# Performance work log

Measured on AMD Instinct MI355X. Metric: run time of the kernel, lower is better.

Reference implementation:

```python
import jax, jax.numpy as jnp
import numpy as np

D_MODEL = 512
N_HEADS = 8
HEAD_DIM = D_MODEL // N_HEADS
BATCH = 2
SEQ = 4096
MAX_SEQ = 4096


def _rope_tables(max_len, dim):
    # freqs = 1/10000^(arange(0,dim,2)/dim); outer(t, freqs); polar -> cos/sin
    inv = 1.0 / (10000.0 ** (np.arange(0, dim, 2, dtype=np.float32) / dim))
    t = np.arange(max_len, dtype=np.float32)
    ang = np.outer(t, inv)  # [max_len, dim/2]
    return jnp.asarray(np.cos(ang)), jnp.asarray(np.sin(ang))


def _apply_rope(x, cos, sin):
    # x: [B, S, H, Hd]; complex-pair rotation over last dim pairs
    B, S, H, Hd = x.shape
    xr = x.reshape(B, S, H, Hd // 2, 2)
    xe, xo = xr[..., 0], xr[..., 1]
    c = cos[:S][None, :, None, :]  # [1,S,1,Hd/2]
    s = sin[:S][None, :, None, :]
    re = xe * c - xo * s
    im = xe * s + xo * c
    return jnp.stack([re, im], axis=-1).reshape(B, S, H, Hd)


def setup_inputs() -> dict:
    key = jax.random.key(0)
    kx, kq, kk, kv, ko = jax.random.split(key, 5)
    std = 1.0 / np.sqrt(D_MODEL)
    return {
        "x": jax.random.normal(kx, (BATCH, SEQ, D_MODEL), dtype=jnp.float32),
        "Wq": jax.random.normal(kq, (D_MODEL, D_MODEL), dtype=jnp.float32) * std,
        "Wk": jax.random.normal(kk, (D_MODEL, D_MODEL), dtype=jnp.float32) * std,
        "Wv": jax.random.normal(kv, (D_MODEL, D_MODEL), dtype=jnp.float32) * std,
        "Wo": jax.random.normal(ko, (D_MODEL, D_MODEL), dtype=jnp.float32) * std,
    }


def reference(x, Wq, Wk, Wv, Wo):
    B, S, D = x.shape
    cos, sin = _rope_tables(MAX_SEQ, HEAD_DIM)
    # nn.Linear: y = x @ W.T
    q = (x @ Wq.T).reshape(B, S, N_HEADS, HEAD_DIM)
    k = (x @ Wk.T).reshape(B, S, N_HEADS, HEAD_DIM)
    v = (x @ Wv.T).reshape(B, S, N_HEADS, HEAD_DIM)
    q = _apply_rope(q, cos, sin)
    k = _apply_rope(k, cos, sin)
    scale = HEAD_DIM ** (-0.5)
    # [B,H,S,S]
    scores = jnp.einsum("bshd,bthd->bhst", q, k) * scale
    causal = jnp.tril(jnp.ones((S, S), dtype=bool))
    scores = jnp.where(causal[None, None], scores, -jnp.inf)
    attn = jax.nn.softmax(scores, axis=-1)
    out = jnp.einsum("bhst,bthd->bshd", attn, v).reshape(B, S, D)
    return out @ Wo.T
```

## Files before the change

kernel.cpp:

```cpp
#include <hip/hip_runtime.h>
#include <hip/hip_bf16.h>
#include <math.h>

#define D_MODEL 512
#define N_HEADS 8
#define HEAD_DIM 64
#define BATCH 2
#define SEQ 4096
#define M_ROWS (BATCH*SEQ)

typedef __attribute__((ext_vector_type(8))) short short8;
typedef __attribute__((ext_vector_type(4))) float f32x4;

__device__ inline short f2bf(float f) {
  union { float f; unsigned u; } v; v.f = f;
  unsigned u = v.u;
  unsigned r = u + 0x7FFFu + ((u >> 16) & 1u);
  return (short)(r >> 16);
}
__device__ inline float bf2f(short s) {
  union { unsigned u; float f; } v; v.u = ((unsigned)(unsigned short)s) << 16;
  return v.f;
}

__device__ inline void gll16(const void* g, void* l) {
  __builtin_amdgcn_global_load_lds(
      (const __attribute__((address_space(1))) unsigned int*)g,
      (__attribute__((address_space(3))) unsigned int*)l, 16, 0, 0);
}

__device__ inline short8 cvt8(float4 a, float4 b) {
  short8 o;
  o[0] = f2bf(a.x); o[1] = f2bf(a.y); o[2] = f2bf(a.z); o[3] = f2bf(a.w);
  o[4] = f2bf(b.x); o[5] = f2bf(b.y); o[6] = f2bf(b.z); o[7] = f2bf(b.w);
  return o;
}

#define XOCT (M_ROWS*D_MODEL/8)
#define WOCT (3*D_MODEL*D_MODEL/8)
#define OOCT (D_MODEL*D_MODEL/8)
__global__ void prep_kernel(const float* __restrict__ x,
                            const float* __restrict__ Wq,
                            const float* __restrict__ Wk,
                            const float* __restrict__ Wv,
                            const float* __restrict__ Wo,
                            short* __restrict__ xb,
                            short* __restrict__ Wqkv,
                            short* __restrict__ Wob,
                            float* __restrict__ cosT,
                            float* __restrict__ sinT) {
  int i = blockIdx.x * blockDim.x + threadIdx.x;
  if (i < XOCT) {
    float4 a = *(const float4*)&x[i * 8];
    float4 b = *(const float4*)&x[i * 8 + 4];
    *(short8*)&xb[i * 8] = cvt8(a, b);
  }
  if (i < WOCT) {
    int e = i * 8;
    int t = e >> 18, r = e & 262143;
    const float* W = (t == 0) ? Wq : ((t == 1) ? Wk : Wv);
    float4 a = *(const float4*)&W[r];
    float4 b = *(const float4*)&W[r + 4];
    *(short8*)&Wqkv[e] = cvt8(a, b);
  }
  if (i < OOCT) {
    float4 a = *(const float4*)&Wo[i * 8];
    float4 b = *(const float4*)&Wo[i * 8 + 4];
    *(short8*)&Wob[i * 8] = cvt8(a, b);
  }
  if (i < SEQ * 32) {
    int s = i >> 5, p = i & 31;
    float e = (float)(2 * p) * (1.0f / 64.0f);
    float inv = powf(10000.0f, -e);
    float ang = (float)s * inv;
    float sv, cv;
    sincosf(ang, &sv, &cv);
    cosT[i] = cv; sinT[i] = sv;
  }
}

template<int MODE>
__global__ __launch_bounds__(256) void gemm_kernel(const short* __restrict__ A,
                                                   const short* __restrict__ B,
                                                   float* __restrict__ out_f,
                                                   short* __restrict__ Qb,
                                                   short* __restrict__ Kb,
                                                   short* __restrict__ Vb,
                                                   const float* __restrict__ cosT,
                                                   const float* __restrict__ sinT) {
  __shared__ short smem[128 * 72 * 2];
  short (*As)[72] = (short(*)[72])smem;
  short (*Bs)[72] = (short(*)[72])(smem + 128 * 72);
  short (*Cs)[136] = (short(*)[136])smem;

  const int m0 = blockIdx.x * 128;
  const int n0 = blockIdx.y * 128;
  const int tid = threadIdx.x;
  const int lane = tid & 63, wid = tid >> 6;
  const int wm = wid >> 1, wn = wid & 1;
  const int l15 = lane & 15, g = lane >> 4;
  const int Kdim = 512;

  f32x4 acc[4][4] = {};

  for (int kt = 0; kt < Kdim; kt += 64) {
    __syncthreads();
    for (int it = 0; it < 4; ++it) {
      int c = it * 256 + tid;
      int row = c >> 3, col = (c & 7) << 3;
      *(short8*)&As[row][col] = *(const short8*)&A[(m0 + row) * Kdim + kt + col];
      *(short8*)&Bs[row][col] = *(const short8*)&B[(n0 + row) * Kdim + kt + col];
    }
    __syncthreads();
    for (int kk = 0; kk < 64; kk += 32) {
      short8 a[4], b[4];
      for (int mi = 0; mi < 4; ++mi)
        a[mi] = *(const short8*)&As[wm * 64 + mi * 16 + l15][kk + (g << 3)];
      for (int ni = 0; ni < 4; ++ni)
        b[ni] = *(const short8*)&Bs[wn * 64 + ni * 16 + l15][kk + (g << 3)];
      for (int mi = 0; mi < 4; ++mi)
        for (int ni = 0; ni < 4; ++ni)
          acc[mi][ni] = __builtin_amdgcn_mfma_f32_16x16x32_bf16(a[mi], b[ni], acc[mi][ni], 0, 0, 0);
    }
  }

  if (MODE == 1) {
    for (int mi = 0; mi < 4; ++mi)
      for (int ni = 0; ni < 4; ++ni)
        for (int r = 0; r < 4; ++r) {
          int row_g = m0 + wm * 64 + mi * 16 + (g << 2) + r;
          int col_g = n0 + wn * 64 + ni * 16 + l15;
          out_f[row_g * 512 + col_g] = acc[mi][ni][r];
        }
    return;
  }

  const int t_blk = n0 >> 9;
  __syncthreads();

  if (t_blk < 2) {
    const float qs = (t_blk == 0) ? 0.18033688011112042f : 1.0f;
    for (int mi = 0; mi < 4; ++mi)
      for (int ni = 0; ni < 4; ++ni)
        for (int r = 0; r < 4; ++r) {
          int lrow = wm * 64 + mi * 16 + (g << 2) + r;
          int ss = (m0 + lrow) & 4095;
          int d = (n0 + wn * 64 + ni * 16 + l15) & 63;
          int p = d >> 1;
          float c = cosT[ss * 32 + p], s = sinT[ss * 32 + p];
          float v = acc[mi][ni][r];
          float partner = __shfl_xor(v, 1);
          float res = (l15 & 1) ? (v * c + partner * s) : (v * c - partner * s);
          Cs[lrow][wn * 64 + ni * 16 + l15] = f2bf(res * qs);
        }
  } else {
    for (int mi = 0; mi < 4; ++mi)
      for (int ni = 0; ni < 4; ++ni)
        for (int r = 0; r < 4; ++r)
          Cs[wm * 64 + mi * 16 + (g << 2) + r][wn * 64 + ni * 16 + l15] =
              f2bf(acc[mi][ni][r]);
  }
  __syncthreads();

  if (t_blk < 2) {
    short* dst = (t_blk == 0) ? Qb : Kb;
#pragma unroll
    for (int it = 0; it < 8; ++it) {
      int row = (tid >> 4) + (it << 4);
      int colb = (tid & 15) << 3;
      short8 vv = *(const short8*)&Cs[row][colb];
      int row_g = m0 + row;
      int ss = row_g & 4095, bb = row_g >> 12;
      int cc = (n0 + colb) & 511;
      int h = cc >> 6, d = cc & 63;
      *(short8*)&dst[(((bb << 3) + h) * SEQ + ss) * 64 + d] = vv;
    }
  } else {
#pragma unroll
    for (int it = 0; it < 8; ++it) {
      int c = tid & 127;
      int sb = ((tid >> 7) << 3) + (it << 4);
      short8 o8;
#pragma unroll
      for (int j = 0; j < 8; ++j) o8[j] = Cs[sb + j][c];
      int row_g0 = m0 + sb;
      int ss = row_g0 & 4095, bb = row_g0 >> 12;
      int cc = (n0 + c) & 511;
      int h = cc >> 6, d = cc & 63;
      *(short8*)&Vb[((long)(((bb << 3) + h) * 64 + d)) * SEQ + ss] = o8;
    }
  }
}

__global__ __launch_bounds__(512, 4) void attn_kernel(const short* __restrict__ Q,
                                                      const short* __restrict__ K,
                                                      const short* __restrict__ Vt,
                                                      short* __restrict__ O) {
  __shared__ short Ks[2][64 * 64];
  __shared__ short Vs[2][64 * 64];
  __shared__ short P_lds[8][16][72];

  const int o = blockIdx.x;
  const int j = o >> 4;
  const int bh = o & 15;
  const int tile = (o < 256) ? (31 - j) : (j - 16);

  const int tid = threadIdx.x, lane = tid & 63, w = tid >> 6;
  const int l15 = lane & 15, g = lane >> 4;
  const long base = (long)bh * SEQ * 64;
  const long baseV = (long)bh * 64 * SEQ;
  const int bb = bh >> 3, h = bh & 7;

  const int srow = tid >> 3;
  const int sc16k = (tid & 7) ^ (srow & 7);
  short* ldsSegK0 = &Ks[0][(tid >> 6) << 9];
  short* ldsSegK1 = &Ks[1][(tid >> 6) << 9];
  short* ldsSegV0 = &Vs[0][(tid >> 6) << 9];
  short* ldsSegV1 = &Vs[1][(tid >> 6) << 9];

  const int q0 = (tile << 7) + (w << 4);
  const int nc = 2 * tile + 2;

  short8 aq0 = *(const short8*)&Q[base + (long)(q0 + l15) * 64 + (g << 3)];
  short8 aq1 = *(const short8*)&Q[base + (long)(q0 + l15) * 64 + 32 + (g << 3)];

  f32x4 o_acc[4] = {};
  float m_r[4], l_r[4];
#pragma unroll
  for (int r = 0; r < 4; ++r) { m_r[r] = -__builtin_inff(); l_r[r] = 0.f; }

  gll16(&K[base + (long)srow * 64 + sc16k * 8], ldsSegK0);
  gll16(&Vt[baseV + (long)srow * SEQ + sc16k * 8], ldsSegV0);

  for (int c = 0; c < nc; ++c) {
    const int kv0 = c << 6;
    const int bi = c & 1;
    __syncthreads();
    if (c + 1 < nc) {
      const int nkv = (c + 1) << 6;
      short* dK = (bi ? ldsSegK0 : ldsSegK1);
      short* dV = (bi ? ldsSegV0 : ldsSegV1);
      gll16(&K[base + (long)(nkv + srow) * 64 + sc16k * 8], dK);
      gll16(&Vt[baseV + (long)srow * SEQ + nkv + sc16k * 8], dV);
    }
    if (kv0 > q0) continue;

    f32x4 sf[4] = {};
    __builtin_amdgcn_s_setprio(1);
#pragma unroll
    for (int f = 0; f < 4; ++f) {
      int row = f * 16 + l15, sw = row & 7;
      short8 bk0 = *(const short8*)&Ks[bi][row * 64 + ((g) ^ sw) * 8];
      short8 bk1 = *(const short8*)&Ks[bi][row * 64 + ((4 + g) ^ sw) * 8];
      sf[f] = __builtin_amdgcn_mfma_f32_16x16x32_bf16(aq0, bk0, sf[f], 0, 0, 0);
      sf[f] = __builtin_amdgcn_mfma_f32_16x16x32_bf16(aq1, bk1, sf[f], 0, 0, 0);
    }
    __builtin_amdgcn_s_setprio(0);
    if (kv0 == (q0 & ~63)) {
#pragma unroll
      for (int f = 0; f < 4; ++f) {
        int kvc = kv0 + f * 16 + l15;
#pragma unroll
        for (int r = 0; r < 4; ++r) {
          int qrow = q0 + (g << 2) + r;
          if (kvc > qrow) sf[f][r] = -__builtin_inff();
        }
      }
    }

    float pmx[4];
#pragma unroll
    for (int r = 0; r < 4; ++r)
      pmx[r] = fmaxf(fmaxf(sf[0][r], sf[1][r]), fmaxf(sf[2][r], sf[3][r]));
    bool ok = (pmx[0] <= m_r[0] + 8.f) && (pmx[1] <= m_r[1] + 8.f) &&
              (pmx[2] <= m_r[2] + 8.f) && (pmx[3] <= m_r[3] + 8.f);
    if (!__all(ok)) {
      float pm[4];
#pragma unroll
      for (int r = 0; r < 4; ++r) pm[r] = pmx[r];
#pragma unroll
      for (int off = 1; off < 16; off <<= 1)
#pragma unroll
        for (int r = 0; r < 4; ++r)
          pm[r] = fmaxf(pm[r], __shfl_xor(pm[r], off));
#pragma unroll
      for (int r = 0; r < 4; ++r) {
        float mn = fmaxf(m_r[r], pm[r]);
        float alpha = exp2f(m_r[r] - mn);
        m_r[r] = mn;
        l_r[r] *= alpha;
#pragma unroll
        for (int db = 0; db < 4; ++db) o_acc[db][r] *= alpha;
      }
    }

    float pr[4][4];
#pragma unroll
    for (int r = 0; r < 4; ++r)
#pragma unroll
      for (int f = 0; f < 4; ++f) {
        float pv = exp2f(sf[f][r] - m_r[r]);
        pr[f][r] = pv;
        l_r[r] += pv;
      }

#pragma unroll
    for (int f = 0; f < 4; ++f)
#pragma unroll
      for (int r = 0; r < 4; ++r)
        P_lds[w][(g << 2) + r][f * 16 + l15] = f2bf(pr[f][r]);

    short8 pa0 = *(const short8*)&P_lds[w][l15][(g << 3)];
    short8 pa1 = *(const short8*)&P_lds[w][l15][32 + (g << 3)];

    __builtin_amdgcn_s_setprio(1);
#pragma unroll
    for (int kk = 0; kk < 2; ++kk) {
      short8 pa = kk ? pa1 : pa0;
#pragma unroll
      for (int db = 0; db < 4; ++db) {
        int row = db * 16 + l15, sw = row & 7;
        short8 bv = *(const short8*)&Vs[bi][row * 64 + ((kk * 4 + g) ^ sw) * 8];
        o_acc[db] = __builtin_amdgcn_mfma_f32_16x16x32_bf16(pa, bv, o_acc[db], 0, 0, 0);
      }
    }
    __builtin_amdgcn_s_setprio(0);
  }

#pragma unroll
  for (int off = 1; off < 16; off <<= 1)
#pragma unroll
    for (int r = 0; r < 4; ++r)
      l_r[r] += __shfl_xor(l_r[r], off);

#pragma unroll
  for (int db = 0; db < 4; ++db)
#pragma unroll
    for (int r = 0; r < 4; ++r) {
      int s_g = q0 + (g << 2) + r;
      float v = o_acc[db][r] / l_r[r];
      O[((long)(bb * SEQ + s_g)) * 512 + h * 64 + db * 16 + l15] = f2bf(v);
    }
}

extern "C" void kernel_launch(void* const* d_in, const int* in_sizes, int n_in,
                              void* d_out, int out_size, void* d_ws, size_t ws_size,
                              hipStream_t stream) {
  const float* x  = (const float*)d_in[0];
  const float* Wq = (const float*)d_in[1];
  const float* Wk = (const float*)d_in[2];
  const float* Wv = (const float*)d_in[3];
  const float* Wo = (const float*)d_in[4];

  char* ws = (char*)d_ws;
  size_t off = 0;
  auto alloc = [&](size_t bytes) {
    void* p = ws + off;
    off += (bytes + 255) & ~(size_t)255;
    return p;
  };
  short* xb   = (short*)alloc((size_t)M_ROWS * 512 * 2);
  short* Wqkv = (short*)alloc((size_t)1536 * 512 * 2);
  short* Wob  = (short*)alloc((size_t)512 * 512 * 2);
  float* cosT = (float*)alloc((size_t)SEQ * 32 * 4);
  float* sinT = (float*)alloc((size_t)SEQ * 32 * 4);
  short* Qb   = (short*)alloc((size_t)16 * SEQ * 64 * 2);
  short* Kb   = (short*)alloc((size_t)16 * SEQ * 64 * 2);
  short* Vt   = (short*)alloc((size_t)16 * SEQ * 64 * 2);
  short* Obuf = (short*)alloc((size_t)M_ROWS * 512 * 2);

  prep_kernel<<<2048, 256, 0, stream>>>(x, Wq, Wk, Wv, Wo, xb, Wqkv, Wob, cosT, sinT);
  gemm_kernel<0><<<dim3(64, 12), 256, 0, stream>>>(xb, Wqkv, nullptr, Qb, Kb, Vt, cosT, sinT);
  attn_kernel<<<512, 512, 0, stream>>>(Qb, Kb, Vt, Obuf);
  gemm_kernel<1><<<dim3(64, 4), 256, 0, stream>>>(Obuf, Wob, (float*)d_out, nullptr, nullptr, nullptr, nullptr, nullptr);
}
```

Before: 208.1 us.

## Transpose score MFMA, keep P in registers, use direct-to-LDS loads in GEMM

The attention kernel swaps the operands of the QK^T MFMA so each lane holds one query row. Row max and sum then need only two cross-lane shuffles, and running stats become scalars per lane. The probability tile is packed with v_cvt_pk_bf16_f32 and rearranged with shuffles instead of a round-trip through P_lds. The projection GEMM now stages A and B tiles with global_load_lds into XOR-swizzled LDS instead of register-staged copies. The cost is extra shuffle instructions for the P relayout and for rescaling with alpha and l.

```diff
diff --git a/kernel.cpp b/kernel.cpp
--- a/kernel.cpp
+++ b/kernel.cpp
@@ -18,9 +18,11 @@
   unsigned r = u + 0x7FFFu + ((u >> 16) & 1u);
   return (short)(r >> 16);
 }
-__device__ inline float bf2f(short s) {
-  union { unsigned u; float f; } v; v.u = ((unsigned)(unsigned short)s) << 16;
-  return v.f;
+
+__device__ inline unsigned cvtpk_bf16(float lo, float hi) {
+  unsigned r;
+  asm("v_cvt_pk_bf16_f32 %0, %1, %2" : "=v"(r) : "v"(lo), "v"(hi));
+  return r;
 }
 
 __device__ inline void gll16(const void* g, void* l) {
@@ -88,9 +90,7 @@
                                                    short* __restrict__ Vb,
                                                    const float* __restrict__ cosT,
                                                    const float* __restrict__ sinT) {
-  __shared__ short smem[128 * 72 * 2];
-  short (*As)[72] = (short(*)[72])smem;
-  short (*Bs)[72] = (short(*)[72])(smem + 128 * 72);
+  __shared__ short smem[18432];
   short (*Cs)[136] = (short(*)[136])smem;
 
   const int m0 = blockIdx.x * 128;
@@ -99,26 +99,38 @@
   const int lane = tid & 63, wid = tid >> 6;
   const int wm = wid >> 1, wn = wid & 1;
   const int l15 = lane & 15, g = lane >> 4;
-  const int Kdim = 512;
+
+  const int srow8 = lane >> 3;
+  const int sblk = (lane & 7) ^ srow8;
 
   f32x4 acc[4][4] = {};
 
-  for (int kt = 0; kt < Kdim; kt += 64) {
+  for (int kt = 0; kt < 512; kt += 64) {
     __syncthreads();
-    for (int it = 0; it < 4; ++it) {
-      int c = it * 256 + tid;
-      int row = c >> 3, col = (c & 7) << 3;
-      *(short8*)&As[row][col] = *(const short8*)&A[(m0 + row) * Kdim + kt + col];
-      *(short8*)&Bs[row][col] = *(const short8*)&B[(n0 + row) * Kdim + kt + col];
+#pragma unroll
+    for (int cc = 0; cc < 4; ++cc) {
+      int r0 = (cc * 4 + wid) * 8;
+      int row = r0 + srow8;
+      gll16(&A[(m0 + row) * 512 + kt + sblk * 8], smem + (cc * 4 + wid) * 512);
+      gll16(&B[(n0 + row) * 512 + kt + sblk * 8], smem + 8192 + (cc * 4 + wid) * 512);
     }
     __syncthreads();
+#pragma unroll
     for (int kk = 0; kk < 64; kk += 32) {
       short8 a[4], b[4];
+#pragma unroll
+      for (int mi = 0; mi < 4; ++mi) {
+        int row = wm * 64 + mi * 16 + l15;
+        a[mi] = *(const short8*)&smem[row * 64 + ((((kk >> 3) + g) ^ (l15 & 7)) << 3)];
+      }
+#pragma unroll
+      for (int ni = 0; ni < 4; ++ni) {
+        int row = wn * 64 + ni * 16 + l15;
+        b[ni] = *(const short8*)&smem[8192 + row * 64 + ((((kk >> 3) + g) ^ (l15 & 7)) << 3)];
+      }
+#pragma unroll
       for (int mi = 0; mi < 4; ++mi)
-        a[mi] = *(const short8*)&As[wm * 64 + mi * 16 + l15][kk + (g << 3)];
-      for (int ni = 0; ni < 4; ++ni)
-        b[ni] = *(const short8*)&Bs[wn * 64 + ni * 16 + l15][kk + (g << 3)];
-      for (int mi = 0; mi < 4; ++mi)
+#pragma unroll
         for (int ni = 0; ni < 4; ++ni)
           acc[mi][ni] = __builtin_amdgcn_mfma_f32_16x16x32_bf16(a[mi], b[ni], acc[mi][ni], 0, 0, 0);
     }
@@ -198,7 +210,6 @@
                                                       short* __restrict__ O) {
   __shared__ short Ks[2][64 * 64];
   __shared__ short Vs[2][64 * 64];
-  __shared__ short P_lds[8][16][72];
 
   const int o = blockIdx.x;
   const int j = o >> 4;
@@ -225,9 +236,7 @@
   short8 aq1 = *(const short8*)&Q[base + (long)(q0 + l15) * 64 + 32 + (g << 3)];
 
   f32x4 o_acc[4] = {};
-  float m_r[4], l_r[4];
-#pragma unroll
-  for (int r = 0; r < 4; ++r) { m_r[r] = -__builtin_inff(); l_r[r] = 0.f; }
+  float m_r = -__builtin_inff(), l_r = 0.f;
 
   gll16(&K[base + (long)srow * 64 + sc16k * 8], ldsSegK0);
   gll16(&Vt[baseV + (long)srow * SEQ + sc16k * 8], ldsSegV0);
@@ -252,66 +261,76 @@
       int row = f * 16 + l15, sw = row & 7;
       short8 bk0 = *(const short8*)&Ks[bi][row * 64 + ((g) ^ sw) * 8];
       short8 bk1 = *(const short8*)&Ks[bi][row * 64 + ((4 + g) ^ sw) * 8];
-      sf[f] = __builtin_amdgcn_mfma_f32_16x16x32_bf16(aq0, bk0, sf[f], 0, 0, 0);
-      sf[f] = __builtin_amdgcn_mfma_f32_16x16x32_bf16(aq1, bk1, sf[f], 0, 0, 0);
+      sf[f] = __builtin_amdgcn_mfma_f32_16x16x32_bf16(bk0, aq0, sf[f], 0, 0, 0);
+      sf[f] = __builtin_amdgcn_mfma_f32_16x16x32_bf16(bk1, aq1, sf[f], 0, 0, 0);
     }
     __builtin_amdgcn_s_setprio(0);
     if (kv0 == (q0 & ~63)) {
-#pragma unroll
-      for (int f = 0; f < 4; ++f) {
-        int kvc = kv0 + f * 16 + l15;
+      int qrow = q0 + l15;
+#pragma unroll
+      for (int f = 0; f < 4; ++f)
 #pragma unroll
         for (int r = 0; r < 4; ++r) {
-          int qrow = q0 + (g << 2) + r;
+          int kvc = kv0 + f * 16 + (g << 2) + r;
           if (kvc > qrow) sf[f][r] = -__builtin_inff();
         }
-      }
-    }
-
-    float pmx[4];
-#pragma unroll
-    for (int r = 0; r < 4; ++r)
-      pmx[r] = fmaxf(fmaxf(sf[0][r], sf[1][r]), fmaxf(sf[2][r], sf[3][r]));
-    bool ok = (pmx[0] <= m_r[0] + 8.f) && (pmx[1] <= m_r[1] + 8.f) &&
-              (pmx[2] <= m_r[2] + 8.f) && (pmx[3] <= m_r[3] + 8.f);
-    if (!__all(ok)) {
-      float pm[4];
-#pragma unroll
-      for (int r = 0; r < 4; ++r) pm[r] = pmx[r];
-#pragma unroll
-      for (int off = 1; off < 16; off <<= 1)
-#pragma unroll
-        for (int r = 0; r < 4; ++r)
-          pm[r] = fmaxf(pm[r], __shfl_xor(pm[r], off));
+    }
+
+    float pmx = sf[0][0];
+#pragma unroll
+    for (int f = 0; f < 4; ++f)
+#pragma unroll
+      for (int r = 0; r < 4; ++r) pmx = fmaxf(pmx, sf[f][r]);
+    if (!__all(pmx <= m_r + 8.f)) {
+      float pm = pmx;
+      pm = fmaxf(pm, __shfl_xor(pm, 16));
+      pm = fmaxf(pm, __shfl_xor(pm, 32));
+      float mn = fmaxf(m_r, pm);
+      float alpha = exp2f(m_r - mn);
+      m_r = mn;
+      l_r *= alpha;
 #pragma unroll
       for (int r = 0; r < 4; ++r) {
-        float mn = fmaxf(m_r[r], pm[r]);
-        float alpha = exp2f(m_r[r] - mn);
-        m_r[r] = mn;
-        l_r[r] *= alpha;
-#pragma unroll
-        for (int db = 0; db < 4; ++db) o_acc[db][r] *= alpha;
+        float ar = __shfl(alpha, (g << 2) + r);
+#pragma unroll
+        for (int db = 0; db < 4; ++db) o_acc[db][r] *= ar;
       }
     }
 
     float pr[4][4];
-#pragma unroll
-    for (int r = 0; r < 4; ++r)
-#pragma unroll
-      for (int f = 0; f < 4; ++f) {
-        float pv = exp2f(sf[f][r] - m_r[r]);
+    float s0 = 0.f;
+#pragma unroll
+    for (int f = 0; f < 4; ++f)
+#pragma unroll
+      for (int r = 0; r < 4; ++r) {
+        float pv = exp2f(sf[f][r] - m_r);
         pr[f][r] = pv;
-        l_r[r] += pv;
-      }
-
-#pragma unroll
-    for (int f = 0; f < 4; ++f)
-#pragma unroll
-      for (int r = 0; r < 4; ++r)
-        P_lds[w][(g << 2) + r][f * 16 + l15] = f2bf(pr[f][r]);
-
-    short8 pa0 = *(const short8*)&P_lds[w][l15][(g << 3)];
-    short8 pa1 = *(const short8*)&P_lds[w][l15][32 + (g << 3)];
+        s0 += pv;
+      }
+    l_r += s0;
+
+    unsigned pk[4][2];
+#pragma unroll
+    for (int f = 0; f < 4; ++f) {
+      pk[f][0] = cvtpk_bf16(pr[f][0], pr[f][1]);
+      pk[f][1] = cvtpk_bf16(pr[f][2], pr[f][3]);
+    }
+    unsigned paw0[4], paw1[4];
+    const bool hi = (g & 2) != 0;
+#pragma unroll
+    for (int w2 = 0; w2 < 4; ++w2) {
+      int srcl = l15 + ((2 * (g & 1) + (w2 >> 1)) << 4);
+      unsigned c0 = (unsigned)__shfl((int)pk[0][w2 & 1], srcl);
+      unsigned c1 = (unsigned)__shfl((int)pk[1][w2 & 1], srcl);
+      unsigned c2 = (unsigned)__shfl((int)pk[2][w2 & 1], srcl);
+      unsigned c3 = (unsigned)__shfl((int)pk[3][w2 & 1], srcl);
+      paw0[w2] = hi ? c1 : c0;
+      paw1[w2] = hi ? c3 : c2;
+    }
+    union { unsigned u[4]; short8 s; } u0, u1;
+#pragma unroll
+    for (int w2 = 0; w2 < 4; ++w2) { u0.u[w2] = paw0[w2]; u1.u[w2] = paw1[w2]; }
+    short8 pa0 = u0.s, pa1 = u1.s;
 
     __builtin_amdgcn_s_setprio(1);
 #pragma unroll
@@ -327,18 +346,15 @@
     __builtin_amdgcn_s_setprio(0);
   }
 
-#pragma unroll
-  for (int off = 1; off < 16; off <<= 1)
-#pragma unroll
-    for (int r = 0; r < 4; ++r)
-      l_r[r] += __shfl_xor(l_r[r], off);
-
+  l_r += __shfl_xor(l_r, 16);
+  l_r += __shfl_xor(l_r, 32);
 #pragma unroll
   for (int db = 0; db < 4; ++db)
 #pragma unroll
     for (int r = 0; r < 4; ++r) {
+      float lq = __shfl(l_r, (g << 2) + r);
       int s_g = q0 + (g << 2) + r;
-      float v = o_acc[db][r] / l_r[r];
+      float v = o_acc[db][r] / lq;
       O[((long)(bb * SEQ + s_g)) * 512 + h * 64 + db * 16 + l15] = f2bf(v);
     }
 }
```

Measured after the change: 206.9 us. About the same (-0.6%).
